# Kernel tuning notes

Measured on AMD Instinct MI355X. Metric: run time of the kernel, lower is better.

Reference implementation:

```python
import jax, jax.numpy as jnp
import numpy as np
import math

D = 1024
L = 4096
B = 4

def setup_inputs() -> dict:
    key = jax.random.key(0)
    ks = jax.random.split(key, 6)
    x = jax.random.normal(ks[0], (B, L, D), dtype=jnp.float32)
    base_phases = jax.random.normal(ks[1], (L, D), dtype=jnp.float32) * math.pi
    s = 1.0 / math.sqrt(D)
    W_v = jax.random.normal(ks[2], (D, D), dtype=jnp.float32) * s
    b_v = jnp.zeros((D,), dtype=jnp.float32)
    ln_g = jnp.ones((D,), dtype=jnp.float32)
    ln_b = jnp.zeros((D,), dtype=jnp.float32)
    W_o = jax.random.normal(ks[3], (D, D), dtype=jnp.float32) * s
    b_o = jnp.zeros((D,), dtype=jnp.float32)
    return {"x": x, "base_phases": base_phases, "W_v": W_v, "b_v": b_v,
            "ln_g": ln_g, "ln_b": ln_b, "W_o": W_o, "b_o": b_o}

def _layernorm(x, g, b, eps=1e-5):
    mu = jnp.mean(x, axis=-1, keepdims=True)
    var = jnp.mean(jnp.square(x - mu), axis=-1, keepdims=True)
    return (x - mu) * jax.lax.rsqrt(var + eps) * g + b

def reference(x, base_phases, W_v, b_v, ln_g, ln_b, W_o, b_o):
    Bv, Lv, Dv = x.shape
    phases = base_phases[:Lv][None, :, :]          # [1, L, D]
    cosp, sinp = jnp.cos(phases), jnp.sin(phases)
    value = jnp.einsum('bld,ed->ble', x, W_v) + b_v  # Linear(D,D)
    mem_real = jnp.cumsum(value * cosp, axis=1)
    mem_imag = jnp.cumsum(value * sinp, axis=1)
    retrieved = (mem_real * cosp + mem_imag * sinp) / math.sqrt(Dv)
    out = jnp.einsum('bld,ed->ble', _layernorm(retrieved, ln_g, ln_b), W_o) + b_o
    return x + out
```

## Files before the change

kernel.cpp:

```cpp
#include <hip/hip_runtime.h>
#include <stdint.h>


#define D_DIM 1024
#define L_DIM 4096
#define B_DIM 4
#define M_DIM (B_DIM * L_DIM)
#define CHUNK 64
#define NCH (L_DIM / CHUNK)
#define NT 16

typedef __attribute__((ext_vector_type(8))) short short8;
typedef __attribute__((ext_vector_type(4))) float f32x4;

__device__ __forceinline__ float bf2f(uint32_t h) {
  union { uint32_t u; float f; } x; x.u = h << 16; return x.f;
}
__device__ __forceinline__ uint16_t f2bf(float f) {
  union { float f; uint32_t u; } x; x.f = f;
  uint32_t u = x.u;
  u += 0x7fffu + ((u >> 16) & 1u);
  return (uint16_t)(u >> 16);
}

__global__ void k_prep(const float* __restrict__ x, const float* __restrict__ Wv,
                       const float* __restrict__ Wo, const float* __restrict__ g,
                       const float* __restrict__ bln, const float* __restrict__ bo,
                       uint16_t* __restrict__ xb, uint16_t* __restrict__ wv,
                       uint16_t* __restrict__ wob, float* __restrict__ u,
                       float* __restrict__ vb) {
  int blk = blockIdx.x;
  int tid = threadIdx.x;
  if (blk < 8192 + 512) {
    const float* in = (blk < 8192) ? x : Wv;
    uint16_t* outp = (blk < 8192) ? xb : wv;
    int base = (blk < 8192) ? blk : (blk - 8192);
    int i = (base * 256 + tid) * 8;
    float4 a = *(const float4*)(in + i);
    float4 b = *(const float4*)(in + i + 4);
    ushort4 o0 = { f2bf(a.x), f2bf(a.y), f2bf(a.z), f2bf(a.w) };
    ushort4 o1 = { f2bf(b.x), f2bf(b.y), f2bf(b.z), f2bf(b.w) };
    *(ushort4*)(outp + i) = o0;
    *(ushort4*)(outp + i + 4) = o1;
    return;
  }
  int e = blk - 8704;
  int d = tid * 4;
  float4 w  = *(const float4*)(Wo + (size_t)e * D_DIM + d);
  float4 gg = *(const float4*)(g + d);
  float4 bb = *(const float4*)(bln + d);
  float gw0 = gg.x * w.x, gw1 = gg.y * w.y, gw2 = gg.z * w.z, gw3 = gg.w * w.w;
  ushort4 o = { f2bf(gw0), f2bf(gw1), f2bf(gw2), f2bf(gw3) };
  *(ushort4*)(wob + (size_t)e * D_DIM + d) = o;
  float su = gw0 + gw1 + gw2 + gw3;
  float sv = bb.x * w.x + bb.y * w.y + bb.z * w.z + bb.w * w.w;
#pragma unroll
  for (int off = 32; off > 0; off >>= 1) {
    su += __shfl_down(su, off);
    sv += __shfl_down(sv, off);
  }
  __shared__ float s1[4], s2[4];
  int wid = tid >> 6, lane = tid & 63;
  if (lane == 0) { s1[wid] = su; s2[wid] = sv; }
  __syncthreads();
  if (tid == 0) {
    u[e]  = s1[0] + s1[1] + s1[2] + s1[3];
    vb[e] = s2[0] + s2[1] + s2[2] + s2[3] + bo[e];
  }
}

template <int MODE>
__global__ __launch_bounds__(512, 2) void k_gemm(
    const uint16_t* __restrict__ A, const uint16_t* __restrict__ W,
    void* __restrict__ outp,
    const float* __restrict__ p0, const float* __restrict__ p1,
    const float* __restrict__ mu, const float* __restrict__ inv,
    const uint16_t* __restrict__ xres) {
  __shared__ char lds[8 * 16384];
  const int tid = threadIdx.x;
  const int lane = tid & 63;
  const int wid = tid >> 6;
  const int wm = wid >> 2;
  const int wn = wid & 3;

  const int idx = blockIdx.x;
  const int bm = (idx & 7) * 8 + ((idx >> 3) >> 2);
  const int bn = (idx >> 3) & 3;

  const int srow = tid >> 3;
  const int scb  = (tid & 7) * 16;
  const int scbs = scb ^ ((srow & 7) << 4);

#define GLL(SRC, DST)                                                            \
  __builtin_amdgcn_global_load_lds((const __attribute__((address_space(1))) void*)(SRC), \
                                   (__attribute__((address_space(3))) void*)(DST), 16, 0, 0)

#define STAGE_A(KS, HA)                                                          \
  do {                                                                           \
    char* _d = lds + ((((KS)&1) * 4 + (HA)) << 14) + tid * 16;                   \
    const char* _s = (const char*)A +                                            \
        (size_t)(bm * 256 + (HA) * 128 + srow) * 2048 + (KS) * 128 + scbs;       \
    GLL(_s, _d);                                                                 \
    GLL(_s + (size_t)64 * 2048, _d + 8192);                                      \
  } while (0)

#define STAGE_B(KS, HB)                                                          \
  do {                                                                           \
    char* _d = lds + ((((KS)&1) * 4 + 2 + (HB)) << 14) + tid * 16;               \
    const char* _s = (const char*)W +                                            \
        (size_t)(bn * 256 + (HB) * 128 + srow) * 2048 + (KS) * 128 + scbs;       \
    GLL(_s, _d);                                                                 \
    GLL(_s + (size_t)64 * 2048, _d + 8192);                                      \
  } while (0)

  const int axor = (lane & 7) << 4;
  const int afr  = lane & 15;
  const int acol = (lane >> 4) * 16;

#define LD_A(PAR, I, KK)                                                         \
  (*(const short8*)(lds + (((PAR) * 4 + wm) << 14) + ((I) * 16 + afr) * 128 +    \
                    (((KK) * 64 + acol) ^ axor)))
#define LD_B(PAR, J, KK)                                                         \
  (*(const short8*)(lds + (((PAR) * 4 + 2 + (wn >> 1)) << 14) +                  \
                    ((wn & 1) * 64 + (J) * 16 + afr) * 128 +                     \
                    (((KK) * 64 + acol) ^ axor)))

#define MFMA(AV, BV, CV) __builtin_amdgcn_mfma_f32_16x16x32_bf16(AV, BV, CV, 0, 0, 0)

  f32x4 acc[8][4];
#pragma unroll
  for (int i = 0; i < 8; ++i)
#pragma unroll
    for (int j = 0; j < 4; ++j)
      acc[i][j] = (f32x4){0.f, 0.f, 0.f, 0.f};

  STAGE_A(0, 0); STAGE_A(0, 1);
  STAGE_B(0, 0); STAGE_B(0, 1);
  STAGE_A(1, 0); STAGE_A(1, 1);
  asm volatile("s_waitcnt vmcnt(4)" ::: "memory");
  __builtin_amdgcn_s_barrier();

  for (int ks = 0; ks < NT; ++ks) {
    const int par = ks & 1;
    short8 A00, A01, A02, A03, A10, A11, A12, A13;
    short8 B00, B01, B02, B03, B10, B11, B12, B13;

    B00 = LD_B(par, 0, 0); B01 = LD_B(par, 1, 0); B02 = LD_B(par, 2, 0); B03 = LD_B(par, 3, 0);
    A00 = LD_A(par, 0, 0); A01 = LD_A(par, 1, 0); A02 = LD_A(par, 2, 0); A03 = LD_A(par, 3, 0);
    __builtin_amdgcn_sched_barrier(0);
    B10 = LD_B(par, 0, 1); B11 = LD_B(par, 1, 1); B12 = LD_B(par, 2, 1); B13 = LD_B(par, 3, 1);
    A10 = LD_A(par, 0, 1); A11 = LD_A(par, 1, 1); A12 = LD_A(par, 2, 1); A13 = LD_A(par, 3, 1);
    __builtin_amdgcn_sched_barrier(0);
    if (ks + 1 < NT) { STAGE_B(ks + 1, 0); STAGE_B(ks + 1, 1); }
    __builtin_amdgcn_s_barrier();
    asm volatile("s_waitcnt lgkmcnt(8)" ::: "memory");
    __builtin_amdgcn_sched_barrier(0);
    __builtin_amdgcn_s_setprio(1);
#pragma unroll
    for (int j = 0; j < 4; ++j) {
      const short8 bj = (j == 0) ? B00 : (j == 1) ? B01 : (j == 2) ? B02 : B03;
      acc[0][j] = MFMA(A00, bj, acc[0][j]);
      acc[1][j] = MFMA(A01, bj, acc[1][j]);
      acc[2][j] = MFMA(A02, bj, acc[2][j]);
      acc[3][j] = MFMA(A03, bj, acc[3][j]);
    }
    asm volatile("s_waitcnt lgkmcnt(0)" ::: "memory");
    __builtin_amdgcn_sched_barrier(0);
#pragma unroll
    for (int j = 0; j < 4; ++j) {
      const short8 bj = (j == 0) ? B10 : (j == 1) ? B11 : (j == 2) ? B12 : B13;
      acc[0][j] = MFMA(A10, bj, acc[0][j]);
      acc[1][j] = MFMA(A11, bj, acc[1][j]);
      acc[2][j] = MFMA(A12, bj, acc[2][j]);
      acc[3][j] = MFMA(A13, bj, acc[3][j]);
    }
    __builtin_amdgcn_s_setprio(0);
    __builtin_amdgcn_s_barrier();

    A00 = LD_A(par, 4, 0); A01 = LD_A(par, 5, 0); A02 = LD_A(par, 6, 0); A03 = LD_A(par, 7, 0);
    __builtin_amdgcn_sched_barrier(0);
    A10 = LD_A(par, 4, 1); A11 = LD_A(par, 5, 1); A12 = LD_A(par, 6, 1); A13 = LD_A(par, 7, 1);
    __builtin_amdgcn_sched_barrier(0);
    asm volatile("s_waitcnt lgkmcnt(4)" ::: "memory");
    __builtin_amdgcn_sched_barrier(0);
    __builtin_amdgcn_s_setprio(1);
#pragma unroll
    for (int j = 0; j < 4; ++j) {
      const short8 bj = (j == 0) ? B00 : (j == 1) ? B01 : (j == 2) ? B02 : B03;
      acc[4][j] = MFMA(A00, bj, acc[4][j]);
      acc[5][j] = MFMA(A01, bj, acc[5][j]);
      acc[6][j] = MFMA(A02, bj, acc[6][j]);
      acc[7][j] = MFMA(A03, bj, acc[7][j]);
    }
    __builtin_amdgcn_s_setprio(0);
    asm volatile("s_waitcnt lgkmcnt(0)" ::: "memory");
    __builtin_amdgcn_sched_barrier(0);
    __builtin_amdgcn_s_barrier();
    __builtin_amdgcn_sched_barrier(0);
    if (ks + 2 < NT) { STAGE_A(ks + 2, 0); STAGE_A(ks + 2, 1); }
    __builtin_amdgcn_s_setprio(1);
#pragma unroll
    for (int j = 0; j < 4; ++j) {
      const short8 bj = (j == 0) ? B10 : (j == 1) ? B11 : (j == 2) ? B12 : B13;
      acc[4][j] = MFMA(A10, bj, acc[4][j]);
      acc[5][j] = MFMA(A11, bj, acc[5][j]);
      acc[6][j] = MFMA(A12, bj, acc[6][j]);
      acc[7][j] = MFMA(A13, bj, acc[7][j]);
    }
    __builtin_amdgcn_s_setprio(0);
    if (ks == NT - 2) { asm volatile("s_waitcnt vmcnt(0)" ::: "memory"); }
    else              { asm volatile("s_waitcnt vmcnt(4)" ::: "memory"); }
    __builtin_amdgcn_s_barrier();
  }

  if (MODE == 0) {
    uint16_t* outv = (uint16_t*)outp;
    __syncthreads();
#pragma unroll
    for (int i = 0; i < 8; ++i)
#pragma unroll
      for (int r = 0; r < 4; ++r) {
        int row = wm * 128 + i * 16 + (lane >> 4) * 4 + r;
#pragma unroll
        for (int j = 0; j < 4; ++j) {
          int ncol = wn * 64 + j * 16 + (lane & 15);
          float v = acc[i][j][r] + p0[bn * 256 + ncol];
          *(uint16_t*)(lds + row * 512 + ((ncol * 2) ^ ((row & 7) << 4))) = f2bf(v);
        }
      }
    __syncthreads();
    {
      int row = tid >> 1, half = tid & 1;
      uint16_t* gdst = outv + (size_t)(bm * 256 + row) * D_DIM + bn * 256 + half * 128;
#pragma unroll
      for (int s = 0; s < 16; ++s) {
        short8 v = *(const short8*)(lds + row * 512 +
                                    ((half * 256 + s * 16) ^ ((row & 7) << 4)));
        *(short8*)(gdst + s * 8) = v;
      }
    }
  } else {
    float* outf = (float*)outp;
#pragma unroll
    for (int i = 0; i < 8; ++i)
#pragma unroll
      for (int r = 0; r < 4; ++r) {
        int m = bm * 256 + wm * 128 + i * 16 + (lane >> 4) * 4 + r;
        float im = inv[m], mm = mu[m];
#pragma unroll
        for (int j = 0; j < 4; ++j) {
          int n = bn * 256 + wn * 64 + j * 16 + (lane & 15);
          outf[(size_t)m * D_DIM + n] =
              im * acc[i][j][r] - im * mm * p0[n] + p1[n] +
              bf2f(xres[(size_t)m * D_DIM + n]);
        }
      }
  }
#undef GLL
#undef STAGE_A
#undef STAGE_B
#undef LD_A
#undef LD_B
#undef MFMA
}

__global__ void k_passA(const uint16_t* __restrict__ value, const float* __restrict__ phases,
                        float* __restrict__ pr, float* __restrict__ pi) {
  int d0 = blockIdx.x * 512 + threadIdx.x * 2;
  int c = blockIdx.y, b = blockIdx.z;
  const uint16_t* vp = value + ((size_t)(b * L_DIM + c * CHUNK)) * D_DIM + d0;
  const float* pp = phases + (size_t)(c * CHUNK) * D_DIM + d0;
  float sr0 = 0, si0 = 0, sr1 = 0, si1 = 0;
#pragma unroll 4
  for (int l = 0; l < CHUNK; ++l) {
    uint32_t vv = *(const uint32_t*)vp; vp += D_DIM;
    float2 ph = *(const float2*)pp; pp += D_DIM;
    float v0 = bf2f(vv & 0xffffu), v1 = bf2f(vv >> 16);
    float s0, c0, s1, c1;
    __sincosf(ph.x, &s0, &c0);
    __sincosf(ph.y, &s1, &c1);
    sr0 += v0 * c0; si0 += v0 * s0;
    sr1 += v1 * c1; si1 += v1 * s1;
  }
  size_t o = ((size_t)b * NCH + c) * D_DIM + d0;
  *(float2*)(pr + o) = make_float2(sr0, sr1);
  *(float2*)(pi + o) = make_float2(si0, si1);
}

__global__ void k_passB(float* __restrict__ pr, float* __restrict__ pi) {
  int d = blockIdx.x * 256 + threadIdx.x;
  int b = blockIdx.y;
  size_t base = (size_t)b * NCH * D_DIM + d;
  float r[NCH], im[NCH];
#pragma unroll
  for (int c = 0; c < NCH; ++c) r[c] = pr[base + (size_t)c * D_DIM];
#pragma unroll
  for (int c = 0; c < NCH; ++c) im[c] = pi[base + (size_t)c * D_DIM];
  float rr = 0, ri = 0;
#pragma unroll
  for (int c = 0; c < NCH; ++c) {
    float t = r[c]; r[c] = rr; rr += t;
    t = im[c]; im[c] = ri; ri += t;
  }
#pragma unroll
  for (int c = 0; c < NCH; ++c) pr[base + (size_t)c * D_DIM] = r[c];
#pragma unroll
  for (int c = 0; c < NCH; ++c) pi[base + (size_t)c * D_DIM] = im[c];
}

__global__ void k_passC(const uint16_t* __restrict__ value, const float* __restrict__ phases,
                        const float* __restrict__ pr, const float* __restrict__ pi,
                        uint16_t* __restrict__ ret) {
  int d0 = blockIdx.x * 512 + threadIdx.x * 2;
  int c = blockIdx.y, b = blockIdx.z;
  size_t o = ((size_t)b * NCH + c) * D_DIM + d0;
  float2 r0 = *(const float2*)(pr + o);
  float2 i0 = *(const float2*)(pi + o);
  float mr0 = r0.x, mr1 = r0.y, mi0 = i0.x, mi1 = i0.y;
  size_t rowoff = ((size_t)(b * L_DIM + c * CHUNK)) * D_DIM + d0;
  const uint16_t* vp = value + rowoff;
  uint16_t* rp = ret + rowoff;
  const float* pp = phases + (size_t)(c * CHUNK) * D_DIM + d0;
  const float isd = 0.03125f;
#pragma unroll 4
  for (int l = 0; l < CHUNK; ++l) {
    uint32_t vv = *(const uint32_t*)vp; vp += D_DIM;
    float2 ph = *(const float2*)pp; pp += D_DIM;
    float v0 = bf2f(vv & 0xffffu), v1 = bf2f(vv >> 16);
    float s0, c0, s1, c1;
    __sincosf(ph.x, &s0, &c0);
    __sincosf(ph.y, &s1, &c1);
    mr0 += v0 * c0; mi0 += v0 * s0;
    mr1 += v1 * c1; mi1 += v1 * s1;
    float o0 = (mr0 * c0 + mi0 * s0) * isd;
    float o1 = (mr1 * c1 + mi1 * s1) * isd;
    *(uint32_t*)rp = (uint32_t)f2bf(o0) | ((uint32_t)f2bf(o1) << 16);
    rp += D_DIM;
  }
}

__global__ void k_stats(const uint16_t* __restrict__ ret, float* __restrict__ mu,
                        float* __restrict__ inv) {
  int m = blockIdx.x, tid = threadIdx.x;
  ushort4 v = *(const ushort4*)(ret + (size_t)m * D_DIM + tid * 4);
  float f0 = bf2f(v.x), f1 = bf2f(v.y), f2_ = bf2f(v.z), f3 = bf2f(v.w);
  float s = f0 + f1 + f2_ + f3;
  float ss = f0 * f0 + f1 * f1 + f2_ * f2_ + f3 * f3;
#pragma unroll
  for (int off = 32; off > 0; off >>= 1) {
    s += __shfl_down(s, off);
    ss += __shfl_down(ss, off);
  }
  __shared__ float a1[4], a2[4];
  int wid = tid >> 6, lane = tid & 63;
  if (lane == 0) { a1[wid] = s; a2[wid] = ss; }
  __syncthreads();
  if (tid == 0) {
    float S = a1[0] + a1[1] + a1[2] + a1[3];
    float SS = a2[0] + a2[1] + a2[2] + a2[3];
    float mm = S * (1.0f / 1024.0f);
    float var = SS * (1.0f / 1024.0f) - mm * mm;
    mu[m] = mm;
    inv[m] = rsqrtf(var + 1e-5f);
  }
}

extern "C" void kernel_launch(void* const* d_in, const int* in_sizes, int n_in,
                              void* d_out, int out_size, void* d_ws, size_t ws_size,
                              hipStream_t stream) {
  const float* x      = (const float*)d_in[0];
  const float* phases = (const float*)d_in[1];
  const float* Wv     = (const float*)d_in[2];
  const float* bv     = (const float*)d_in[3];
  const float* lng    = (const float*)d_in[4];
  const float* lnb    = (const float*)d_in[5];
  const float* Wo     = (const float*)d_in[6];
  const float* bo     = (const float*)d_in[7];
  float* out = (float*)d_out;

  char* ws = (char*)d_ws;
  uint16_t* xb    = (uint16_t*)(ws);
  uint16_t* value = (uint16_t*)(ws + (32ull << 20));
  uint16_t* wv    = (uint16_t*)(ws + (64ull << 20));
  uint16_t* wob   = (uint16_t*)(ws + (66ull << 20));
  float* pr       = (float*)(ws + (68ull << 20));
  float* pi       = (float*)(ws + (69ull << 20));
  float* u        = (float*)(ws + (70ull << 20));
  float* vb       = (float*)(ws + (70ull << 20) + 4096);
  float* mu       = (float*)(ws + (71ull << 20));
  float* inv      = (float*)(ws + (72ull << 20));
  uint16_t* retr  = value;

  k_prep<<<8192 + 512 + 1024, 256, 0, stream>>>(x, Wv, Wo, lng, lnb, bo,
                                                xb, wv, wob, u, vb);
  k_gemm<0><<<(M_DIM / 256) * (D_DIM / 256), 512, 0, stream>>>(
      xb, wv, value, bv, nullptr, nullptr, nullptr, nullptr);
  k_passA<<<dim3(2, NCH, B_DIM), 256, 0, stream>>>(value, phases, pr, pi);
  k_passB<<<dim3(D_DIM / 256, B_DIM), 256, 0, stream>>>(pr, pi);
  k_passC<<<dim3(2, NCH, B_DIM), 256, 0, stream>>>(value, phases, pr, pi, retr);
  k_stats<<<M_DIM, 256, 0, stream>>>(retr, mu, inv);
  k_gemm<1><<<(M_DIM / 256) * (D_DIM / 256), 512, 0, stream>>>(
      retr, wob, out, u, vb, mu, inv, xb);
}
```

Baseline: 146.8 us.

## Restructure GEMM main loop into four phases with finer-grained global staging

Reorganises the bf16 MFMA GEMM K-loop from two half-phases with 16 live fragment registers into four phases, each loading four A and four B fragments, and interleaves the next tile's global-to-LDS stages (B half 0, B half 1, A half 0, A half 1) between phases. The prefetch depth for A drops from two tiles ahead to one, and wait counts change accordingly. This is meant to cut register pressure and spread memory issue more evenly across compute. The cost is more barriers per iteration and less latency hiding for A loads.

```diff
diff --git a/kernel.cpp b/kernel.cpp
--- a/kernel.cpp
+++ b/kernel.cpp
@@ -126,6 +126,7 @@
                     (((KK) * 64 + acol) ^ axor)))
 
 #define MFMA(AV, BV, CV) __builtin_amdgcn_mfma_f32_16x16x32_bf16(AV, BV, CV, 0, 0, 0)
+#define SB0() __builtin_amdgcn_sched_barrier(0)
 
   f32x4 acc[8][4];
 #pragma unroll
@@ -134,82 +135,90 @@
     for (int j = 0; j < 4; ++j)
       acc[i][j] = (f32x4){0.f, 0.f, 0.f, 0.f};
 
+  STAGE_B(0, 0); STAGE_B(0, 1);
   STAGE_A(0, 0); STAGE_A(0, 1);
-  STAGE_B(0, 0); STAGE_B(0, 1);
-  STAGE_A(1, 0); STAGE_A(1, 1);
-  asm volatile("s_waitcnt vmcnt(4)" ::: "memory");
+  asm volatile("s_waitcnt vmcnt(2)" ::: "memory");
   __builtin_amdgcn_s_barrier();
 
   for (int ks = 0; ks < NT; ++ks) {
     const int par = ks & 1;
-    short8 A00, A01, A02, A03, A10, A11, A12, A13;
-    short8 B00, B01, B02, B03, B10, B11, B12, B13;
-
-    B00 = LD_B(par, 0, 0); B01 = LD_B(par, 1, 0); B02 = LD_B(par, 2, 0); B03 = LD_B(par, 3, 0);
-    A00 = LD_A(par, 0, 0); A01 = LD_A(par, 1, 0); A02 = LD_A(par, 2, 0); A03 = LD_A(par, 3, 0);
-    __builtin_amdgcn_sched_barrier(0);
-    B10 = LD_B(par, 0, 1); B11 = LD_B(par, 1, 1); B12 = LD_B(par, 2, 1); B13 = LD_B(par, 3, 1);
-    A10 = LD_A(par, 0, 1); A11 = LD_A(par, 1, 1); A12 = LD_A(par, 2, 1); A13 = LD_A(par, 3, 1);
-    __builtin_amdgcn_sched_barrier(0);
-    if (ks + 1 < NT) { STAGE_B(ks + 1, 0); STAGE_B(ks + 1, 1); }
-    __builtin_amdgcn_s_barrier();
-    asm volatile("s_waitcnt lgkmcnt(8)" ::: "memory");
-    __builtin_amdgcn_sched_barrier(0);
+    short8 Af0, Af1, Af2, Af3, Bf0, Bf1, Bf2, Bf3;
+
+    Bf0 = LD_B(par, 0, 0); Bf1 = LD_B(par, 1, 0); Bf2 = LD_B(par, 2, 0); Bf3 = LD_B(par, 3, 0);
+    Af0 = LD_A(par, 0, 0); Af1 = LD_A(par, 1, 0); Af2 = LD_A(par, 2, 0); Af3 = LD_A(par, 3, 0);
+    SB0();
+    if (ks + 1 < NT) STAGE_B(ks + 1, 0);
+    __builtin_amdgcn_s_barrier();
+    asm volatile("s_waitcnt lgkmcnt(0)" ::: "memory");
+    SB0();
     __builtin_amdgcn_s_setprio(1);
 #pragma unroll
     for (int j = 0; j < 4; ++j) {
-      const short8 bj = (j == 0) ? B00 : (j == 1) ? B01 : (j == 2) ? B02 : B03;
-      acc[0][j] = MFMA(A00, bj, acc[0][j]);
-      acc[1][j] = MFMA(A01, bj, acc[1][j]);
-      acc[2][j] = MFMA(A02, bj, acc[2][j]);
-      acc[3][j] = MFMA(A03, bj, acc[3][j]);
-    }
-    asm volatile("s_waitcnt lgkmcnt(0)" ::: "memory");
-    __builtin_amdgcn_sched_barrier(0);
-#pragma unroll
-    for (int j = 0; j < 4; ++j) {
-      const short8 bj = (j == 0) ? B10 : (j == 1) ? B11 : (j == 2) ? B12 : B13;
-      acc[0][j] = MFMA(A10, bj, acc[0][j]);
-      acc[1][j] = MFMA(A11, bj, acc[1][j]);
-      acc[2][j] = MFMA(A12, bj, acc[2][j]);
-      acc[3][j] = MFMA(A13, bj, acc[3][j]);
+      const short8 bj = (j == 0) ? Bf0 : (j == 1) ? Bf1 : (j == 2) ? Bf2 : Bf3;
+      acc[0][j] = MFMA(Af0, bj, acc[0][j]);
+      acc[1][j] = MFMA(Af1, bj, acc[1][j]);
+      acc[2][j] = MFMA(Af2, bj, acc[2][j]);
+      acc[3][j] = MFMA(Af3, bj, acc[3][j]);
     }
     __builtin_amdgcn_s_setprio(0);
-    __builtin_amdgcn_s_barrier();
-
-    A00 = LD_A(par, 4, 0); A01 = LD_A(par, 5, 0); A02 = LD_A(par, 6, 0); A03 = LD_A(par, 7, 0);
-    __builtin_amdgcn_sched_barrier(0);
-    A10 = LD_A(par, 4, 1); A11 = LD_A(par, 5, 1); A12 = LD_A(par, 6, 1); A13 = LD_A(par, 7, 1);
-    __builtin_amdgcn_sched_barrier(0);
-    asm volatile("s_waitcnt lgkmcnt(4)" ::: "memory");
-    __builtin_amdgcn_sched_barrier(0);
+    if (ks == NT - 1) { asm volatile("s_waitcnt vmcnt(0)" ::: "memory"); }
+    else              { asm volatile("s_waitcnt vmcnt(2)" ::: "memory"); }
+    __builtin_amdgcn_s_barrier();
+
+    Af0 = LD_A(par, 4, 0); Af1 = LD_A(par, 5, 0); Af2 = LD_A(par, 6, 0); Af3 = LD_A(par, 7, 0);
+    SB0();
+    if (ks + 1 < NT) STAGE_B(ks + 1, 1);
+    __builtin_amdgcn_s_barrier();
+    asm volatile("s_waitcnt lgkmcnt(0)" ::: "memory");
+    SB0();
     __builtin_amdgcn_s_setprio(1);
 #pragma unroll
     for (int j = 0; j < 4; ++j) {
-      const short8 bj = (j == 0) ? B00 : (j == 1) ? B01 : (j == 2) ? B02 : B03;
-      acc[4][j] = MFMA(A00, bj, acc[4][j]);
-      acc[5][j] = MFMA(A01, bj, acc[5][j]);
-      acc[6][j] = MFMA(A02, bj, acc[6][j]);
-      acc[7][j] = MFMA(A03, bj, acc[7][j]);
+      const short8 bj = (j == 0) ? Bf0 : (j == 1) ? Bf1 : (j == 2) ? Bf2 : Bf3;
+      acc[4][j] = MFMA(Af0, bj, acc[4][j]);
+      acc[5][j] = MFMA(Af1, bj, acc[5][j]);
+      acc[6][j] = MFMA(Af2, bj, acc[6][j]);
+      acc[7][j] = MFMA(Af3, bj, acc[7][j]);
     }
     __builtin_amdgcn_s_setprio(0);
+    __builtin_amdgcn_s_barrier();
+
+    Bf0 = LD_B(par, 0, 1); Bf1 = LD_B(par, 1, 1); Bf2 = LD_B(par, 2, 1); Bf3 = LD_B(par, 3, 1);
+    Af0 = LD_A(par, 0, 1); Af1 = LD_A(par, 1, 1); Af2 = LD_A(par, 2, 1); Af3 = LD_A(par, 3, 1);
+    SB0();
+    if (ks + 1 < NT) STAGE_A(ks + 1, 0);
+    __builtin_amdgcn_s_barrier();
     asm volatile("s_waitcnt lgkmcnt(0)" ::: "memory");
-    __builtin_amdgcn_sched_barrier(0);
-    __builtin_amdgcn_s_barrier();
-    __builtin_amdgcn_sched_barrier(0);
-    if (ks + 2 < NT) { STAGE_A(ks + 2, 0); STAGE_A(ks + 2, 1); }
+    SB0();
     __builtin_amdgcn_s_setprio(1);
 #pragma unroll
     for (int j = 0; j < 4; ++j) {
-      const short8 bj = (j == 0) ? B10 : (j == 1) ? B11 : (j == 2) ? B12 : B13;
-      acc[4][j] = MFMA(A10, bj, acc[4][j]);
-      acc[5][j] = MFMA(A11, bj, acc[5][j]);
-      acc[6][j] = MFMA(A12, bj, acc[6][j]);
-      acc[7][j] = MFMA(A13, bj, acc[7][j]);
+      const short8 bj = (j == 0) ? Bf0 : (j == 1) ? Bf1 : (j == 2) ? Bf2 : Bf3;
+      acc[0][j] = MFMA(Af0, bj, acc[0][j]);
+      acc[1][j] = MFMA(Af1, bj, acc[1][j]);
+      acc[2][j] = MFMA(Af2, bj, acc[2][j]);
+      acc[3][j] = MFMA(Af3, bj, acc[3][j]);
     }
     __builtin_amdgcn_s_setprio(0);
-    if (ks == NT - 2) { asm volatile("s_waitcnt vmcnt(0)" ::: "memory"); }
-    else              { asm volatile("s_waitcnt vmcnt(4)" ::: "memory"); }
+    __builtin_amdgcn_s_barrier();
+
+    Af0 = LD_A(par, 4, 1); Af1 = LD_A(par, 5, 1); Af2 = LD_A(par, 6, 1); Af3 = LD_A(par, 7, 1);
+    SB0();
+    if (ks + 1 < NT) STAGE_A(ks + 1, 1);
+    __builtin_amdgcn_s_barrier();
+    asm volatile("s_waitcnt lgkmcnt(0)" ::: "memory");
+    SB0();
+    __builtin_amdgcn_s_setprio(1);
+#pragma unroll
+    for (int j = 0; j < 4; ++j) {
+      const short8 bj = (j == 0) ? Bf0 : (j == 1) ? Bf1 : (j == 2) ? Bf2 : Bf3;
+      acc[4][j] = MFMA(Af0, bj, acc[4][j]);
+      acc[5][j] = MFMA(Af1, bj, acc[5][j]);
+      acc[6][j] = MFMA(Af2, bj, acc[6][j]);
+      acc[7][j] = MFMA(Af3, bj, acc[7][j]);
+    }
+    __builtin_amdgcn_s_setprio(0);
+    if (ks < NT - 1) { asm volatile("s_waitcnt vmcnt(2)" ::: "memory"); }
     __builtin_amdgcn_s_barrier();
   }
 
@@ -262,6 +271,7 @@
 #undef LD_A
 #undef LD_B
 #undef MFMA
+#undef SB0
 }
 
 __global__ void k_passA(const uint16_t* __restrict__ value, const float* __restrict__ phases,
```

After: 148.7 us. No clear change (+1.3%).
